# Optimization experiments

Measured on AMD Instinct MI355X. Metric: run time of the kernel, lower is better.

Reference implementation:

```python
import jax, jax.numpy as jnp
import numpy as np

D = 1152      # hidden_size
H = 16        # num_heads
DH = D // H   # head_dim = 72
NCHUNK = 8    # images
L = 1024      # tokens per image (32x32 patches)
S = NCHUNK * L


def rotate_half(x):
    x1, x2 = jnp.split(x, 2, axis=-1)
    return jnp.concatenate([-x2, x1], axis=-1)


def setup_inputs() -> dict:
    key = jax.random.key(0)
    k0, k1, k2, k3, k4 = jax.random.split(key, 5)
    hidden_states = jax.random.normal(k0, (S, D), dtype=jnp.float32)
    qkv_w = jax.random.normal(k1, (3 * D, D), dtype=jnp.float32) * 0.02
    qkv_b = jax.random.normal(k2, (3 * D,), dtype=jnp.float32) * 0.02
    proj_w = jax.random.normal(k3, (D, D), dtype=jnp.float32) * 0.02
    proj_b = jax.random.normal(k4, (D,), dtype=jnp.float32) * 0.02
    # vision RoPE tables: [S, head_dim] with duplicated half-frequencies
    pos = jnp.arange(S, dtype=jnp.float32)
    inv_freq = 1.0 / (10000.0 ** (jnp.arange(0, DH, 2, dtype=jnp.float32) / DH))
    freqs = jnp.outer(pos, inv_freq)              # [S, DH//2]
    emb = jnp.concatenate([freqs, freqs], -1)     # [S, DH]
    cos, sin = jnp.cos(emb), jnp.sin(emb)
    cu_seqlens = jnp.arange(NCHUNK + 1, dtype=jnp.int32) * L
    return dict(hidden_states=hidden_states, cos=cos, sin=sin,
                qkv_w=qkv_w, qkv_b=qkv_b, proj_w=proj_w, proj_b=proj_b,
                cu_seqlens=cu_seqlens)


def reference(hidden_states, cos, sin, qkv_w, qkv_b, proj_w, proj_b, cu_seqlens):
    seq = hidden_states.shape[0]
    num_heads = H
    head_dim = qkv_w.shape[0] // (3 * num_heads)
    # fused QKV projection (torch Linear: x @ W^T + b)
    qkv = hidden_states @ qkv_w.T + qkv_b                 # [S, 3D]
    qkv = qkv.reshape(seq, 3, num_heads, head_dim)
    q, k, v = qkv[:, 0], qkv[:, 1], qkv[:, 2]             # [S, H, DH]
    # RoPE in fp32, broadcast cos/sin over heads
    c = cos[:, None, :].astype(jnp.float32)
    s = sin[:, None, :].astype(jnp.float32)
    qf, kf = q.astype(jnp.float32), k.astype(jnp.float32)
    q = (qf * c + rotate_half(qf) * s).astype(q.dtype)
    k = (kf * c + rotate_half(kf) * s).astype(k.dtype)
    # cu_seqlens defines equal-length segments -> vectorize over chunks
    cu = np.asarray(cu_seqlens)
    chunk = int(cu[1] - cu[0])
    n = seq // chunk
    qc = q.reshape(n, chunk, num_heads, head_dim)
    kc = k.reshape(n, chunk, num_heads, head_dim)
    vc = v.reshape(n, chunk, num_heads, head_dim)
    scale = head_dim ** -0.5
    attn = jnp.einsum('nqhd,nkhd->nhqk', qc, kc) * scale  # [n,H,L,L]
    attn = jax.nn.softmax(attn.astype(jnp.float32), axis=-1).astype(q.dtype)
    out = jnp.einsum('nhqk,nkhd->nqhd', attn, vc)         # [n,L,H,DH]
    out = out.reshape(seq, num_heads * head_dim)
    return out @ proj_w.T + proj_b
```

## Files before the change

### kernel.cpp

```cpp
#include <hip/hip_runtime.h>
#include <stdint.h>

typedef unsigned short ushort_t;
typedef short bf16x8 __attribute__((ext_vector_type(8)));
typedef float f32x4 __attribute__((ext_vector_type(4)));
typedef ushort_t us2 __attribute__((ext_vector_type(2)));
typedef ushort_t us4 __attribute__((ext_vector_type(4)));
typedef ushort_t us8 __attribute__((ext_vector_type(8)));

__device__ __forceinline__ float b2f(ushort_t u) {
    union { unsigned int i; float f; } v; v.i = ((unsigned int)u) << 16; return v.f;
}
__device__ __forceinline__ ushort_t f2b(float f) {
    union { float f; unsigned int i; } v; v.f = f;
    unsigned int r = v.i + 0x7fffu + ((v.i >> 16) & 1u);
    return (ushort_t)(r >> 16);
}

typedef __attribute__((address_space(3))) unsigned int lds_u32;
typedef __attribute__((address_space(1))) const unsigned int gbl_u32;

__device__ __forceinline__ void gload_lds16(const void* g, void* l) {
    __builtin_amdgcn_global_load_lds((gbl_u32*)g, (lds_u32*)l, 16, 0, 0);
}

__global__ void cvt_f32_bf16(const float* __restrict__ src, ushort_t* __restrict__ dst, int n8)
{
    const int i = blockIdx.x * 256 + threadIdx.x;
    if (i >= n8) return;
    f32x4 a = *(const f32x4*)&src[i * 8];
    f32x4 b = *(const f32x4*)&src[i * 8 + 4];
    us8 o;
#pragma unroll
    for (int j = 0; j < 4; j++) { o[j] = f2b(a[j]); o[j + 4] = f2b(b[j]); }
    *(us8*)&dst[i * 8] = o;
}

template <bool OUT_F32>
__global__ __launch_bounds__(256, 4) void gemm_bt_bias(
    const ushort_t* __restrict__ A, const ushort_t* __restrict__ B,
    const float* __restrict__ bias, void* __restrict__ Cv,
    int M, int N, int K)
{
    __shared__ short Sm[16384];

    const int t = threadIdx.x;
    const int lane = t & 63, w = t >> 6;
    const int qd = lane >> 4, ln = lane & 15;
    const int wm = w >> 1, wn = w & 1;
    const int m0 = blockIdx.y * 128, n0 = blockIdx.x * 128;
    const int KITER = K >> 5;

    f32x4 acc[4][4];
#pragma unroll
    for (int i = 0; i < 4; i++)
#pragma unroll
        for (int j = 0; j < 4; j++) acc[i][j] = (f32x4){0.f, 0.f, 0.f, 0.f};

    const int rA = t >> 2;
    const int colSw = ((t & 3) ^ (rA & 3)) * 8;
    const ushort_t* gA  = A + (size_t)(m0 + rA) * K + colSw;
    const ushort_t* gA2 = A + (size_t)(m0 + 64 + rA) * K + colSw;
    const ushort_t* gB  = B + (size_t)(n0 + rA) * K + colSw;
    const ushort_t* gB2 = B + (size_t)(n0 + 64 + rA) * K + colSw;

    gload_lds16(gA,  Sm + t * 8);
    gload_lds16(gA2, Sm + (t + 256) * 8);
    gload_lds16(gB,  Sm + 8192 + t * 8);
    gload_lds16(gB2, Sm + 8192 + (t + 256) * 8);

    const int pc = (qd ^ (ln & 3)) * 8;

    for (int kt = 0; kt < KITER; kt++) {
        __syncthreads();
        if (kt + 1 < KITER) {
            const int k1 = (kt + 1) << 5;
            const int nbo = ((kt + 1) & 1) * 4096;
            gload_lds16(gA + k1,  Sm + nbo + t * 8);
            gload_lds16(gA2 + k1, Sm + nbo + (t + 256) * 8);
            gload_lds16(gB + k1,  Sm + 8192 + nbo + t * 8);
            gload_lds16(gB2 + k1, Sm + 8192 + nbo + (t + 256) * 8);
        }
        const int cbo = (kt & 1) * 4096;
        const short* AsB = Sm + cbo;
        const short* BsB = Sm + 8192 + cbo;

        bf16x8 af[4], bfv[4];
#pragma unroll
        for (int i = 0; i < 4; i++)
            af[i] = *(const bf16x8*)&AsB[(wm * 64 + i * 16 + ln) * 32 + pc];
#pragma unroll
        for (int j = 0; j < 4; j++)
            bfv[j] = *(const bf16x8*)&BsB[(wn * 64 + j * 16 + ln) * 32 + pc];
#pragma unroll
        for (int i = 0; i < 4; i++)
#pragma unroll
            for (int j = 0; j < 4; j++)
                acc[i][j] = __builtin_amdgcn_mfma_f32_16x16x32_bf16(
                    af[i], bfv[j], acc[i][j], 0, 0, 0);
    }

    float bv[4];
#pragma unroll
    for (int j = 0; j < 4; j++) bv[j] = bias[n0 + wn * 64 + j * 16 + ln];

    if (!OUT_F32) {
        __syncthreads();
        ushort_t* Ct = (ushort_t*)Cv;
#pragma unroll
        for (int i = 0; i < 4; i++)
#pragma unroll
            for (int j = 0; j < 4; j++)
#pragma unroll
                for (int r = 0; r < 4; r++)
                    Sm[(wm * 64 + i * 16 + qd * 4 + r) * 128 + wn * 64 + j * 16 + ln] =
                        (short)f2b(acc[i][j][r] + bv[j]);
        __syncthreads();
#pragma unroll
        for (int q = 0; q < 8; q++) {
            const int c = t + q * 256;
            const int row = c >> 4, cc = c & 15;
            *(us8*)&Ct[(size_t)(m0 + row) * N + n0 + cc * 8] =
                *(const us8*)&Sm[row * 128 + cc * 8];
        }
    } else {
        float* Ct = (float*)Cv;
        float* Cf = (float*)Sm;
#pragma unroll
        for (int p = 0; p < 2; p++) {
            __syncthreads();
            if (wm == p) {
#pragma unroll
                for (int i = 0; i < 4; i++)
#pragma unroll
                    for (int j = 0; j < 4; j++)
#pragma unroll
                        for (int r = 0; r < 4; r++)
                            Cf[(i * 16 + qd * 4 + r) * 128 + wn * 64 + j * 16 + ln] =
                                acc[i][j][r] + bv[j];
            }
            __syncthreads();
#pragma unroll
            for (int q = 0; q < 8; q++) {
                const int c = t + q * 256;
                const int row = c >> 5, cc = c & 31;
                *(f32x4*)&Ct[(size_t)(m0 + p * 64 + row) * N + n0 + cc * 4] =
                    *(const f32x4*)&Cf[row * 128 + cc * 4];
            }
        }
    }
}

__global__ void rope_qk(ushort_t* __restrict__ qkv,
                        const float* __restrict__ cosb,
                        const float* __restrict__ sinb,
                        ushort_t* __restrict__ kb)
{
    const int idx = blockIdx.x * 256 + threadIdx.x;
    const int d0c = idx % 9;
    const int h = (idx / 9) & 15;
    const int s = idx / 144;
    const int d0 = d0c * 4;
    const int n = s >> 10, l = s & 1023;
    const size_t src = (size_t)s * 3456 + h * 72;
    const size_t dstrow = ((size_t)(n * 16 + h) * 1024 + l) * 128;

    f32x4 c1 = *(const f32x4*)&cosb[s * 72 + d0];
    f32x4 c2 = *(const f32x4*)&cosb[s * 72 + d0 + 36];
    f32x4 s1 = *(const f32x4*)&sinb[s * 72 + d0];
    f32x4 s2 = *(const f32x4*)&sinb[s * 72 + d0 + 36];

    {
        us4 x1 = *(const us4*)&qkv[src + d0];
        us4 x2 = *(const us4*)&qkv[src + d0 + 36];
        us4 o1, o2;
#pragma unroll
        for (int j = 0; j < 4; j++) {
            float a = b2f(x1[j]), b = b2f(x2[j]);
            o1[j] = f2b(a * c1[j] - b * s1[j]);
            o2[j] = f2b(b * c2[j] + a * s2[j]);
        }
        *(us4*)&qkv[src + d0] = o1;
        *(us4*)&qkv[src + d0 + 36] = o2;
    }
    {
        us4 x1 = *(const us4*)&qkv[src + 1152 + d0];
        us4 x2 = *(const us4*)&qkv[src + 1152 + d0 + 36];
        us4 o1, o2;
#pragma unroll
        for (int j = 0; j < 4; j++) {
            float a = b2f(x1[j]), b = b2f(x2[j]);
            o1[j] = f2b(a * c1[j] - b * s1[j]);
            o2[j] = f2b(b * c2[j] + a * s2[j]);
        }
        *(us4*)&kb[dstrow + d0] = o1;
        *(us4*)&kb[dstrow + d0 + 36] = o2;
    }
    if (d0c < 7) {
        us8 z = (us8){0, 0, 0, 0, 0, 0, 0, 0};
        *(us8*)&kb[dstrow + 72 + d0c * 8] = z;
    }
}

__global__ void v_transpose(const ushort_t* __restrict__ qkv, ushort_t* __restrict__ vt)
{
    __shared__ short T[64 * 80];
    const int t = threadIdx.x;
    const int nh = blockIdx.x >> 4, kvb = blockIdx.x & 15;
    const int h = nh & 15, n = nh >> 4;
    const int s0 = n * 1024 + kvb * 64;

#pragma unroll
    for (int i = 0; i < 3; i++) {
        int c = t + i * 256;
        if (c < 576) {
            int row = c / 9, off = (c % 9) * 8;
            *(us8*)&T[row * 80 + off] =
                *(const us8*)&qkv[(size_t)(s0 + row) * 3456 + 2304 + h * 72 + off];
        }
    }
    __syncthreads();

#pragma unroll
    for (int i = 0; i < 3; i++) {
        int c = t + i * 256;
        if (c < 640) {
            int d = c >> 3, kc = c & 7;
            us8 o;
            if (d < 72) {
#pragma unroll
                for (int j = 0; j < 8; j++) o[j] = (ushort_t)T[(kc * 8 + j) * 80 + d];
            } else {
                o = (us8){0, 0, 0, 0, 0, 0, 0, 0};
            }
            *(us8*)&vt[((size_t)nh * 80 + d) * 1024 + kvb * 64 + kc * 8] = o;
        }
    }
}

__global__ __launch_bounds__(256, 2) void flash_attn(
    const ushort_t* __restrict__ qkv, const ushort_t* __restrict__ kb,
    const ushort_t* __restrict__ vt, ushort_t* __restrict__ ob)
{
    __shared__ short Ks[2][64 * 128];
    __shared__ short VtS[2][80 * 64];
    __shared__ short Ps[4][32 * 72];

    const int t = threadIdx.x;
    const int lane = t & 63, w = t >> 6;
    const int qd = lane >> 4, ln = lane & 15;
    const int lnx = ln & 7;
    const int nh = blockIdx.x >> 3, qt = blockIdx.x & 7;
    const int q0 = qt * 128;
    const int h = nh & 15, n = nh >> 4;
    const float scale = 0.11785113019775793f;

    const ushort_t* kbase = kb + (size_t)nh * 1024 * 128;
    const ushort_t* vbase = vt + (size_t)nh * 80 * 1024;

    bf16x8 qf[2][3];
    {
        const ushort_t* qsrc = qkv + (size_t)(n * 1024 + q0 + w * 32) * 3456 + h * 72;
#pragma unroll
        for (int im = 0; im < 2; im++)
#pragma unroll
            for (int ks = 0; ks < 3; ks++)
                qf[im][ks] = *(const bf16x8*)&qsrc[(size_t)(im * 16 + ln) * 3456 + ks * 32 + qd * 8];
    }

#pragma unroll
    for (int i = 0; i < 4; i++) {
        int c = t + i * 256, r = c >> 4, kc = c & 15;
        gload_lds16(kbase + (size_t)r * 128 + (kc ^ (r & 7)) * 8, &Ks[0][c * 8]);
    }
#pragma unroll
    for (int i = 0; i < 3; i++) {
        int c = t + i * 256;
        if (c < 640) {
            int d = c >> 3, kc = c & 7;
            gload_lds16(vbase + (size_t)d * 1024 + (kc ^ (d & 7)) * 8, &VtS[0][c * 8]);
        }
    }

    float l_lane[2][4];
    f32x4 acc_o[2][5];
#pragma unroll
    for (int im = 0; im < 2; im++) {
#pragma unroll
        for (int r = 0; r < 4; r++) l_lane[im][r] = 0.f;
#pragma unroll
        for (int jn = 0; jn < 5; jn++) acc_o[im][jn] = (f32x4){0.f, 0.f, 0.f, 0.f};
    }

    for (int it = 0; it < 16; it++) {
        __syncthreads();

        if (it < 15) {
            const int nb = (it + 1) & 1;
            const ushort_t* knext = kbase + (size_t)(it + 1) * 8192;
#pragma unroll
            for (int i = 0; i < 4; i++) {
                int c = t + i * 256, r = c >> 4, kc = c & 15;
                gload_lds16(knext + (size_t)r * 128 + (kc ^ (r & 7)) * 8, &Ks[nb][c * 8]);
            }
            const ushort_t* vnext = vbase + (it + 1) * 64;
#pragma unroll
            for (int i = 0; i < 3; i++) {
                int c = t + i * 256;
                if (c < 640) {
                    int d = c >> 3, kc = c & 7;
                    gload_lds16(vnext + (size_t)d * 1024 + (kc ^ (d & 7)) * 8, &VtS[nb][c * 8]);
                }
            }
        }

        const short* KsB = Ks[it & 1];
        const short* VtB = VtS[it & 1];

        f32x4 sc[2][4];
#pragma unroll
        for (int im = 0; im < 2; im++)
#pragma unroll
            for (int jk = 0; jk < 4; jk++) sc[im][jk] = (f32x4){0.f, 0.f, 0.f, 0.f};
#pragma unroll
        for (int ks = 0; ks < 3; ks++) {
            const int m = ks * 4 + qd;
#pragma unroll
            for (int jk = 0; jk < 4; jk++) {
                bf16x8 bfr = *(const bf16x8*)&KsB[(jk * 16 + ln) * 128 + (m ^ lnx) * 8];
                sc[0][jk] = __builtin_amdgcn_mfma_f32_16x16x32_bf16(qf[0][ks], bfr, sc[0][jk], 0, 0, 0);
                sc[1][jk] = __builtin_amdgcn_mfma_f32_16x16x32_bf16(qf[1][ks], bfr, sc[1][jk], 0, 0, 0);
            }
        }

#pragma unroll
        for (int im = 0; im < 2; im++) {
#pragma unroll
            for (int r = 0; r < 4; r++) {
                float p0 = __expf(sc[im][0][r] * scale);
                float p1 = __expf(sc[im][1][r] * scale);
                float p2 = __expf(sc[im][2][r] * scale);
                float p3 = __expf(sc[im][3][r] * scale);
                l_lane[im][r] += (p0 + p1) + (p2 + p3);
                short* pd = &Ps[w][(im * 16 + qd * 4 + r) * 72 + ln];
                pd[0]  = (short)f2b(p0);
                pd[16] = (short)f2b(p1);
                pd[32] = (short)f2b(p2);
                pd[48] = (short)f2b(p3);
            }
        }

#pragma unroll
        for (int ks = 0; ks < 2; ks++) {
            const int m = ks * 4 + qd;
            bf16x8 p0f = *(const bf16x8*)&Ps[w][(ln) * 72 + ks * 32 + qd * 8];
            bf16x8 p1f = *(const bf16x8*)&Ps[w][(16 + ln) * 72 + ks * 32 + qd * 8];
#pragma unroll
            for (int jn = 0; jn < 5; jn++) {
                bf16x8 vf = *(const bf16x8*)&VtB[(jn * 16 + ln) * 64 + (m ^ lnx) * 8];
                acc_o[0][jn] = __builtin_amdgcn_mfma_f32_16x16x32_bf16(p0f, vf, acc_o[0][jn], 0, 0, 0);
                acc_o[1][jn] = __builtin_amdgcn_mfma_f32_16x16x32_bf16(p1f, vf, acc_o[1][jn], 0, 0, 0);
            }
        }
    }

    const size_t obase = ((size_t)(n * 1024 + q0)) * 1152 + h * 72;
#pragma unroll
    for (int im = 0; im < 2; im++) {
#pragma unroll
        for (int r = 0; r < 4; r++) {
            float l = l_lane[im][r];
            l += __shfl_xor(l, 1);
            l += __shfl_xor(l, 2);
            l += __shfl_xor(l, 4);
            l += __shfl_xor(l, 8);
            const float inv = 1.0f / l;
            const int rowl = w * 32 + im * 16 + qd * 4 + r;
#pragma unroll
            for (int jn = 0; jn < 5; jn++) {
                const int d = jn * 16 + ln;
                if (d < 72)
                    ob[obase + (size_t)rowl * 1152 + d] = f2b(acc_o[im][jn][r] * inv);
            }
        }
    }
}

extern "C" void kernel_launch(void* const* d_in, const int* in_sizes, int n_in,
                              void* d_out, int out_size, void* d_ws, size_t ws_size,
                              hipStream_t stream)
{
    const float* hs     = (const float*)d_in[0];
    const float* cosb   = (const float*)d_in[1];
    const float* sinb   = (const float*)d_in[2];
    const float* qkv_w  = (const float*)d_in[3];
    const float* qkv_b  = (const float*)d_in[4];
    const float* proj_w = (const float*)d_in[5];
    const float* proj_b = (const float*)d_in[6];

    char* ws = (char*)d_ws;
    ushort_t* hs_bf   = (ushort_t*)(ws);
    ushort_t* attn    = (ushort_t*)(ws);
    ushort_t* qkvw_bf = (ushort_t*)(ws + 18874368);
    ushort_t* projw_bf= (ushort_t*)(ws + 26836992);
    ushort_t* qkv_tmp = (ushort_t*)(ws + 29491200);
    ushort_t* k_buf   = (ushort_t*)(ws + 86114304);
    ushort_t* v_t     = (ushort_t*)(ws + 119668736);
    float*    out     = (float*)d_out;

    cvt_f32_bf16<<<4608, 256, 0, stream>>>(hs, hs_bf, 9437184 / 8);
    cvt_f32_bf16<<<1944, 256, 0, stream>>>(qkv_w, qkvw_bf, 3981312 / 8);
    cvt_f32_bf16<<<648, 256, 0, stream>>>(proj_w, projw_bf, 1327104 / 8);

    gemm_bt_bias<false><<<dim3(27, 64), 256, 0, stream>>>(hs_bf, qkvw_bf, qkv_b, qkv_tmp, 8192, 3456, 1152);
    rope_qk<<<4608, 256, 0, stream>>>(qkv_tmp, cosb, sinb, k_buf);
    v_transpose<<<2048, 256, 0, stream>>>(qkv_tmp, v_t);
    flash_attn<<<1024, 256, 0, stream>>>(qkv_tmp, k_buf, v_t, attn);
    gemm_bt_bias<true><<<dim3(9, 64), 256, 0, stream>>>(attn, projw_bf, proj_b, out, 8192, 1152, 1152);
}
```

Before: 364.1 us.

## Retile flash attention to 64 query rows per wave with 32-key tiles

Flash attention now has each wave handle 64 query rows (256 per block, 512 blocks) and step through keys in 32-wide tiles, so every K/V fragment read from LDS feeds four MFMAs instead of two. The P and V^T staging buffers shrink and their swizzle changes to (ln>>1)&3. The GEMM LDS swizzle pattern is changed in the same way to cut bank conflicts. In exchange the kernel holds more accumulator registers and runs twice as many loop iterations, each with a barrier. It also launches only 512 blocks, which lowers occupancy and the number of blocks the hardware can overlap.

```diff
diff --git a/kernel.cpp b/kernel.cpp
--- a/kernel.cpp
+++ b/kernel.cpp
@@ -58,7 +58,7 @@
         for (int j = 0; j < 4; j++) acc[i][j] = (f32x4){0.f, 0.f, 0.f, 0.f};
 
     const int rA = t >> 2;
-    const int colSw = ((t & 3) ^ (rA & 3)) * 8;
+    const int colSw = ((t & 3) ^ ((rA >> 1) & 3)) * 8;
     const ushort_t* gA  = A + (size_t)(m0 + rA) * K + colSw;
     const ushort_t* gA2 = A + (size_t)(m0 + 64 + rA) * K + colSw;
     const ushort_t* gB  = B + (size_t)(n0 + rA) * K + colSw;
@@ -69,7 +69,7 @@
     gload_lds16(gB,  Sm + 8192 + t * 8);
     gload_lds16(gB2, Sm + 8192 + (t + 256) * 8);
 
-    const int pc = (qd ^ (ln & 3)) * 8;
+    const int pc = (qd ^ ((ln >> 1) & 3)) * 8;
 
     for (int kt = 0; kt < KITER; kt++) {
         __syncthreads();
@@ -242,74 +242,75 @@
     const ushort_t* __restrict__ qkv, const ushort_t* __restrict__ kb,
     const ushort_t* __restrict__ vt, ushort_t* __restrict__ ob)
 {
-    __shared__ short Ks[2][64 * 128];
-    __shared__ short VtS[2][80 * 64];
-    __shared__ short Ps[4][32 * 72];
+    __shared__ short Ks[2][32 * 128];
+    __shared__ short VtS[2][80 * 32];
+    __shared__ short Ps[4][64 * 40];
 
     const int t = threadIdx.x;
     const int lane = t & 63, w = t >> 6;
     const int qd = lane >> 4, ln = lane & 15;
     const int lnx = ln & 7;
-    const int nh = blockIdx.x >> 3, qt = blockIdx.x & 7;
-    const int q0 = qt * 128;
+    const int lns = (ln >> 1) & 3;
+    const int nh = blockIdx.x >> 2, qt = blockIdx.x & 3;
+    const int q0 = qt * 256;
     const int h = nh & 15, n = nh >> 4;
     const float scale = 0.11785113019775793f;
 
     const ushort_t* kbase = kb + (size_t)nh * 1024 * 128;
     const ushort_t* vbase = vt + (size_t)nh * 80 * 1024;
 
-    bf16x8 qf[2][3];
+    bf16x8 qf[4][3];
     {
-        const ushort_t* qsrc = qkv + (size_t)(n * 1024 + q0 + w * 32) * 3456 + h * 72;
-#pragma unroll
-        for (int im = 0; im < 2; im++)
+        const ushort_t* qsrc = qkv + (size_t)(n * 1024 + q0 + w * 64) * 3456 + h * 72;
+#pragma unroll
+        for (int im = 0; im < 4; im++)
 #pragma unroll
             for (int ks = 0; ks < 3; ks++)
                 qf[im][ks] = *(const bf16x8*)&qsrc[(size_t)(im * 16 + ln) * 3456 + ks * 32 + qd * 8];
     }
 
 #pragma unroll
-    for (int i = 0; i < 4; i++) {
+    for (int i = 0; i < 2; i++) {
         int c = t + i * 256, r = c >> 4, kc = c & 15;
         gload_lds16(kbase + (size_t)r * 128 + (kc ^ (r & 7)) * 8, &Ks[0][c * 8]);
     }
-#pragma unroll
-    for (int i = 0; i < 3; i++) {
-        int c = t + i * 256;
-        if (c < 640) {
-            int d = c >> 3, kc = c & 7;
-            gload_lds16(vbase + (size_t)d * 1024 + (kc ^ (d & 7)) * 8, &VtS[0][c * 8]);
-        }
-    }
-
-    float l_lane[2][4];
-    f32x4 acc_o[2][5];
-#pragma unroll
-    for (int im = 0; im < 2; im++) {
+    {
+        int c = t, d = c >> 2, kc = c & 3;
+        gload_lds16(vbase + (size_t)d * 1024 + (kc ^ ((d >> 1) & 3)) * 8, &VtS[0][c * 8]);
+        if (t < 64) {
+            int c2 = t + 256, d2 = c2 >> 2, kc2 = c2 & 3;
+            gload_lds16(vbase + (size_t)d2 * 1024 + (kc2 ^ ((d2 >> 1) & 3)) * 8, &VtS[0][c2 * 8]);
+        }
+    }
+
+    float l_lane[4][4];
+    f32x4 acc_o[4][5];
+#pragma unroll
+    for (int im = 0; im < 4; im++) {
 #pragma unroll
         for (int r = 0; r < 4; r++) l_lane[im][r] = 0.f;
 #pragma unroll
         for (int jn = 0; jn < 5; jn++) acc_o[im][jn] = (f32x4){0.f, 0.f, 0.f, 0.f};
     }
 
-    for (int it = 0; it < 16; it++) {
+    for (int it = 0; it < 32; it++) {
         __syncthreads();
 
-        if (it < 15) {
+        if (it < 31) {
             const int nb = (it + 1) & 1;
-            const ushort_t* knext = kbase + (size_t)(it + 1) * 8192;
-#pragma unroll
-            for (int i = 0; i < 4; i++) {
+            const ushort_t* knext = kbase + (size_t)(it + 1) * 4096;
+#pragma unroll
+            for (int i = 0; i < 2; i++) {
                 int c = t + i * 256, r = c >> 4, kc = c & 15;
                 gload_lds16(knext + (size_t)r * 128 + (kc ^ (r & 7)) * 8, &Ks[nb][c * 8]);
             }
-            const ushort_t* vnext = vbase + (it + 1) * 64;
-#pragma unroll
-            for (int i = 0; i < 3; i++) {
-                int c = t + i * 256;
-                if (c < 640) {
-                    int d = c >> 3, kc = c & 7;
-                    gload_lds16(vnext + (size_t)d * 1024 + (kc ^ (d & 7)) * 8, &VtS[nb][c * 8]);
+            const ushort_t* vnext = vbase + (it + 1) * 32;
+            {
+                int c = t, d = c >> 2, kc = c & 3;
+                gload_lds16(vnext + (size_t)d * 1024 + (kc ^ ((d >> 1) & 3)) * 8, &VtS[nb][c * 8]);
+                if (t < 64) {
+                    int c2 = t + 256, d2 = c2 >> 2, kc2 = c2 & 3;
+                    gload_lds16(vnext + (size_t)d2 * 1024 + (kc2 ^ ((d2 >> 1) & 3)) * 8, &VtS[nb][c2 * 8]);
                 }
             }
         }
@@ -317,56 +318,52 @@
         const short* KsB = Ks[it & 1];
         const short* VtB = VtS[it & 1];
 
-        f32x4 sc[2][4];
-#pragma unroll
-        for (int im = 0; im < 2; im++)
-#pragma unroll
-            for (int jk = 0; jk < 4; jk++) sc[im][jk] = (f32x4){0.f, 0.f, 0.f, 0.f};
+        f32x4 sc[4][2];
+#pragma unroll
+        for (int im = 0; im < 4; im++)
+#pragma unroll
+            for (int jk = 0; jk < 2; jk++) sc[im][jk] = (f32x4){0.f, 0.f, 0.f, 0.f};
 #pragma unroll
         for (int ks = 0; ks < 3; ks++) {
             const int m = ks * 4 + qd;
 #pragma unroll
-            for (int jk = 0; jk < 4; jk++) {
+            for (int jk = 0; jk < 2; jk++) {
                 bf16x8 bfr = *(const bf16x8*)&KsB[(jk * 16 + ln) * 128 + (m ^ lnx) * 8];
-                sc[0][jk] = __builtin_amdgcn_mfma_f32_16x16x32_bf16(qf[0][ks], bfr, sc[0][jk], 0, 0, 0);
-                sc[1][jk] = __builtin_amdgcn_mfma_f32_16x16x32_bf16(qf[1][ks], bfr, sc[1][jk], 0, 0, 0);
-            }
-        }
-
-#pragma unroll
-        for (int im = 0; im < 2; im++) {
+#pragma unroll
+                for (int im = 0; im < 4; im++)
+                    sc[im][jk] = __builtin_amdgcn_mfma_f32_16x16x32_bf16(
+                        qf[im][ks], bfr, sc[im][jk], 0, 0, 0);
+            }
+        }
+
+#pragma unroll
+        for (int im = 0; im < 4; im++) {
 #pragma unroll
             for (int r = 0; r < 4; r++) {
                 float p0 = __expf(sc[im][0][r] * scale);
                 float p1 = __expf(sc[im][1][r] * scale);
-                float p2 = __expf(sc[im][2][r] * scale);
-                float p3 = __expf(sc[im][3][r] * scale);
-                l_lane[im][r] += (p0 + p1) + (p2 + p3);
-                short* pd = &Ps[w][(im * 16 + qd * 4 + r) * 72 + ln];
+                l_lane[im][r] += p0 + p1;
+                short* pd = &Ps[w][(im * 16 + qd * 4 + r) * 40 + ln];
                 pd[0]  = (short)f2b(p0);
                 pd[16] = (short)f2b(p1);
-                pd[32] = (short)f2b(p2);
-                pd[48] = (short)f2b(p3);
-            }
-        }
-
-#pragma unroll
-        for (int ks = 0; ks < 2; ks++) {
-            const int m = ks * 4 + qd;
-            bf16x8 p0f = *(const bf16x8*)&Ps[w][(ln) * 72 + ks * 32 + qd * 8];
-            bf16x8 p1f = *(const bf16x8*)&Ps[w][(16 + ln) * 72 + ks * 32 + qd * 8];
-#pragma unroll
-            for (int jn = 0; jn < 5; jn++) {
-                bf16x8 vf = *(const bf16x8*)&VtB[(jn * 16 + ln) * 64 + (m ^ lnx) * 8];
-                acc_o[0][jn] = __builtin_amdgcn_mfma_f32_16x16x32_bf16(p0f, vf, acc_o[0][jn], 0, 0, 0);
-                acc_o[1][jn] = __builtin_amdgcn_mfma_f32_16x16x32_bf16(p1f, vf, acc_o[1][jn], 0, 0, 0);
-            }
-        }
-    }
-
-    const size_t obase = ((size_t)(n * 1024 + q0)) * 1152 + h * 72;
-#pragma unroll
-    for (int im = 0; im < 2; im++) {
+            }
+        }
+
+#pragma unroll
+        for (int jn = 0; jn < 5; jn++) {
+            bf16x8 vf = *(const bf16x8*)&VtB[(jn * 16 + ln) * 32 + (qd ^ lns) * 8];
+#pragma unroll
+            for (int im = 0; im < 4; im++) {
+                bf16x8 pf = *(const bf16x8*)&Ps[w][(im * 16 + ln) * 40 + qd * 8];
+                acc_o[im][jn] = __builtin_amdgcn_mfma_f32_16x16x32_bf16(
+                    pf, vf, acc_o[im][jn], 0, 0, 0);
+            }
+        }
+    }
+
+    const size_t obase = ((size_t)(n * 1024 + q0 + w * 64)) * 1152 + h * 72;
+#pragma unroll
+    for (int im = 0; im < 4; im++) {
 #pragma unroll
         for (int r = 0; r < 4; r++) {
             float l = l_lane[im][r];
@@ -375,7 +372,7 @@
             l += __shfl_xor(l, 4);
             l += __shfl_xor(l, 8);
             const float inv = 1.0f / l;
-            const int rowl = w * 32 + im * 16 + qd * 4 + r;
+            const int rowl = im * 16 + qd * 4 + r;
 #pragma unroll
             for (int jn = 0; jn < 5; jn++) {
                 const int d = jn * 16 + ln;
@@ -415,6 +412,6 @@
     gemm_bt_bias<false><<<dim3(27, 64), 256, 0, stream>>>(hs_bf, qkvw_bf, qkv_b, qkv_tmp, 8192, 3456, 1152);
     rope_qk<<<4608, 256, 0, stream>>>(qkv_tmp, cosb, sinb, k_buf);
     v_transpose<<<2048, 256, 0, stream>>>(qkv_tmp, v_t);
-    flash_attn<<<1024, 256, 0, stream>>>(qkv_tmp, k_buf, v_t, attn);
+    flash_attn<<<512, 256, 0, stream>>>(qkv_tmp, k_buf, v_t, attn);
     gemm_bt_bias<true><<<dim3(9, 64), 256, 0, stream>>>(attn, projw_bf, proj_b, out, 8192, 1152, 1152);
 }
```

Result: faster. 355.1 us (-2.5%).
